# Optimization experiments

Hardware: AMD Instinct MI355X
Metric: run time of the kernel (lower is better)

## Reference

```python
import jax, jax.numpy as jnp
import numpy as np

NEG_INF = jnp.finfo(jnp.float32).min


def setup_inputs() -> dict:
    key = jax.random.key(0)
    ks = jax.random.split(key, 8)
    B, C, V = 64, 2048, 256
    ART = 2048
    D = C + ART        # 4096, classifier input
    F = 4096           # feature_size
    OUT = 1000         # out_channels
    x = jax.random.normal(ks[0], (B, C, V), dtype=jnp.float32)
    x_art = jax.random.normal(ks[1], (B, ART, V), dtype=jnp.float32)
    list_length = jax.random.randint(ks[2], (B,), 1, V + 1, dtype=jnp.int32)
    w1 = jax.random.normal(ks[3], (D, F), dtype=jnp.float32) * 0.02
    b1 = jnp.zeros((F,), dtype=jnp.float32)
    w2 = jax.random.normal(ks[4], (F, F), dtype=jnp.float32) * 0.02
    b2 = jnp.zeros((F,), dtype=jnp.float32)
    w3 = jax.random.normal(ks[5], (F, OUT), dtype=jnp.float32) * 0.02
    b3 = jnp.zeros((OUT,), dtype=jnp.float32)
    return {"x": x, "x_art": x_art, "list_length": list_length,
            "w1": w1, "b1": b1, "w2": w2, "b2": b2, "w3": w3, "b3": b3}


def reference(x, x_art, list_length, w1, b1, w2, b2, w3, b3):
    # x: [B, C, V], x_art: [B, ART, V] -> feats [B, V, C+ART]
    feats = jnp.concatenate((jnp.swapaxes(x, 1, 2), jnp.swapaxes(x_art, 1, 2)), axis=-1)
    B, V, D = feats.shape
    # Ragged max over views: view 0 is always included in the torch loop,
    # so effective length = max(list_length, 1).
    lens = jnp.maximum(list_length, 1)
    mask = jnp.arange(V, dtype=jnp.int32)[None, :] < lens[:, None]  # [B, V]
    pooled = jnp.max(jnp.where(mask[:, :, None], feats, NEG_INF), axis=1)  # [B, D]
    # Classifier MLP (dropout is identity at inference)
    h = jax.nn.relu(pooled @ w1 + b1)
    h = jax.nn.relu(h @ w2 + b2)
    return h @ w3 + b3
```

## Files before the change

### kernel.cpp

```cpp
#include <hip/hip_runtime.h>
#include <cfloat>

#define BB 64
#define CC 2048
#define AR 2048
#define DD 4096
#define VV 256
#define FF 4096
#define OO 1000

__global__ __launch_bounds__(256) void pool_kernel(
    const float* __restrict__ x, const float* __restrict__ xart,
    const int* __restrict__ ll, float* __restrict__ pooledT)
{
    int waveId = (blockIdx.x * 256 + threadIdx.x) >> 6;
    int lane   = threadIdx.x & 63;
    int row0   = waveId * 32;
    int b  = row0 >> 12;
    int d0 = row0 & 4095;
    int len = ll[b];
    if (len < 1) len = 1;
    const float* base = (d0 < CC)
        ? (x    + ((size_t)b * CC + d0)        * VV)
        : (xart + ((size_t)b * AR + (d0 - CC)) * VV);
    int v0  = lane * 4;
    int rem = len - v0;

    for (int r = 0; r < 32; r += 4) {
        const float* s = base + (size_t)r * VV;
        float m0 = -FLT_MAX, m1 = -FLT_MAX, m2 = -FLT_MAX, m3 = -FLT_MAX;
        if (rem > 0) {
            float4 a0 = *(const float4*)(s + v0);
            float4 a1 = *(const float4*)(s + VV + v0);
            float4 a2 = *(const float4*)(s + 2 * VV + v0);
            float4 a3 = *(const float4*)(s + 3 * VV + v0);
            m0 = a0.x; m1 = a1.x; m2 = a2.x; m3 = a3.x;
            if (rem > 1) { m0 = fmaxf(m0, a0.y); m1 = fmaxf(m1, a1.y);
                           m2 = fmaxf(m2, a2.y); m3 = fmaxf(m3, a3.y); }
            if (rem > 2) { m0 = fmaxf(m0, a0.z); m1 = fmaxf(m1, a1.z);
                           m2 = fmaxf(m2, a2.z); m3 = fmaxf(m3, a3.z); }
            if (rem > 3) { m0 = fmaxf(m0, a0.w); m1 = fmaxf(m1, a1.w);
                           m2 = fmaxf(m2, a2.w); m3 = fmaxf(m3, a3.w); }
        }
        #pragma unroll
        for (int off = 32; off > 0; off >>= 1) {
            m0 = fmaxf(m0, __shfl_xor(m0, off, 64));
            m1 = fmaxf(m1, __shfl_xor(m1, off, 64));
            m2 = fmaxf(m2, __shfl_xor(m2, off, 64));
            m3 = fmaxf(m3, __shfl_xor(m3, off, 64));
        }
        float wv = m0;
        if (lane == 1) wv = m1;
        else if (lane == 2) wv = m2;
        else if (lane == 3) wv = m3;
        if (lane < 4)
            pooledT[(size_t)(d0 + r + lane) * 64 + b] = wv;
    }
}

__global__ __launch_bounds__(256) void gemm_partial(
    const float* __restrict__ P, const float* __restrict__ W,
    float* __restrict__ part, int F, int kchunk)
{
    __shared__ float lds_p[16][64];
    __shared__ float lds_w[16][128];
    int t  = threadIdx.x;
    int tx = t & 15, ty = t >> 4;
    int f0 = blockIdx.x * 128;
    int k0 = blockIdx.y * kchunk;
    int stages = kchunk >> 4;
    int c1 = f0 + tx * 4;
    int c2 = f0 + 64 + tx * 4;
    bool v2 = (c2 + 3 < F) || (c2 + 4 == F);

    float acc[4][8];
    #pragma unroll
    for (int i = 0; i < 4; ++i)
        #pragma unroll
        for (int j = 0; j < 8; ++j) acc[i][j] = 0.f;

    int k = k0 + ty;
    float4 pv  = *(const float4*)(P + (size_t)k * 64 + tx * 4);
    const float* wr = W + (size_t)k * F;
    float4 wv0 = *(const float4*)(wr + c1);
    float4 wv1;
    if (v2) wv1 = *(const float4*)(wr + c2);
    else {
        wv1.x = (c2     < F) ? wr[c2]     : 0.f;
        wv1.y = (c2 + 1 < F) ? wr[c2 + 1] : 0.f;
        wv1.z = (c2 + 2 < F) ? wr[c2 + 2] : 0.f;
        wv1.w = (c2 + 3 < F) ? wr[c2 + 3] : 0.f;
    }

    for (int s = 0; s < stages; ++s) {
        __syncthreads();
        *(float4*)&lds_p[ty][tx * 4]      = pv;
        *(float4*)&lds_w[ty][tx * 4]      = wv0;
        *(float4*)&lds_w[ty][64 + tx * 4] = wv1;
        __syncthreads();
        if (s + 1 < stages) {
            int kn = k0 + (s + 1) * 16 + ty;
            pv = *(const float4*)(P + (size_t)kn * 64 + tx * 4);
            const float* wrn = W + (size_t)kn * F;
            wv0 = *(const float4*)(wrn + c1);
            if (v2) wv1 = *(const float4*)(wrn + c2);
            else {
                wv1.x = (c2     < F) ? wrn[c2]     : 0.f;
                wv1.y = (c2 + 1 < F) ? wrn[c2 + 1] : 0.f;
                wv1.z = (c2 + 2 < F) ? wrn[c2 + 2] : 0.f;
                wv1.w = (c2 + 3 < F) ? wrn[c2 + 3] : 0.f;
            }
        }
        #pragma unroll
        for (int kk = 0; kk < 16; ++kk) {
            float4 p4 = *(const float4*)&lds_p[kk][ty * 4];
            float4 wa = *(const float4*)&lds_w[kk][tx * 4];
            float4 wb = *(const float4*)&lds_w[kk][64 + tx * 4];
            #pragma unroll
            for (int i = 0; i < 4; ++i) {
                float pi = (i == 0) ? p4.x : (i == 1) ? p4.y : (i == 2) ? p4.z : p4.w;
                acc[i][0] += pi * wa.x;  acc[i][1] += pi * wa.y;
                acc[i][2] += pi * wa.z;  acc[i][3] += pi * wa.w;
                acc[i][4] += pi * wb.x;  acc[i][5] += pi * wb.y;
                acc[i][6] += pi * wb.z;  acc[i][7] += pi * wb.w;
            }
        }
    }

    float* dst = part + (size_t)(blockIdx.y * 64) * F;
    #pragma unroll
    for (int i = 0; i < 4; ++i) {
        float* r = dst + (size_t)(ty * 4 + i) * F;
        *(float4*)(r + c1) = make_float4(acc[i][0], acc[i][1], acc[i][2], acc[i][3]);
        if (v2)
            *(float4*)(r + c2) = make_float4(acc[i][4], acc[i][5], acc[i][6], acc[i][7]);
        else {
            if (c2     < F) r[c2]     = acc[i][4];
            if (c2 + 1 < F) r[c2 + 1] = acc[i][5];
            if (c2 + 2 < F) r[c2 + 2] = acc[i][6];
            if (c2 + 3 < F) r[c2 + 3] = acc[i][7];
        }
    }
}

__global__ __launch_bounds__(256) void reduce_bias_relu_T(
    const float* __restrict__ part, const float* __restrict__ bias,
    float* __restrict__ outT, int nchunk, int F)
{
    __shared__ float lds[64 * 17];
    int t  = threadIdx.x;
    int f0 = blockIdx.x * 16;
    int fl = t & 15;
    int ty = t >> 4;
    float bv = bias[f0 + fl];
    float acc[4];
    #pragma unroll
    for (int j = 0; j < 4; ++j) acc[j] = bv;
    for (int c = 0; c < nchunk; ++c) {
        const float* p = part + ((size_t)c * 64) * F + f0 + fl;
        #pragma unroll
        for (int j = 0; j < 4; ++j) {
            int b = j * 16 + ty;
            acc[j] += p[(size_t)b * F];
        }
    }
    #pragma unroll
    for (int j = 0; j < 4; ++j) {
        int b = j * 16 + ty;
        lds[b * 17 + fl] = fmaxf(acc[j], 0.f);
    }
    __syncthreads();
    #pragma unroll
    for (int j = 0; j < 4; ++j) {
        int idx = j * 256 + t;
        int f = idx >> 6;
        int b = idx & 63;
        outT[(size_t)(f0 + f) * 64 + b] = lds[b * 17 + f];
    }
}

__global__ __launch_bounds__(256) void reduce_out_kernel(
    const float* __restrict__ part, const float* __restrict__ bias,
    float* __restrict__ out, int nchunk)
{
    int idx = blockIdx.x * 256 + threadIdx.x;
    if (idx >= BB * OO) return;
    int b = idx / OO, f = idx - b * OO;
    float v = bias[f];
    const float* p = part + (size_t)b * OO + f;
    #pragma unroll 8
    for (int c = 0; c < nchunk; ++c)
        v += p[(size_t)c * 64 * OO];
    out[idx] = v;
}

extern "C" void kernel_launch(void* const* d_in, const int* in_sizes, int n_in,
                              void* d_out, int out_size, void* d_ws, size_t ws_size,
                              hipStream_t stream) {
    const float* x    = (const float*)d_in[0];
    const float* xart = (const float*)d_in[1];
    const int*   ll   = (const int*)d_in[2];
    const float* w1   = (const float*)d_in[3];
    const float* b1   = (const float*)d_in[4];
    const float* w2   = (const float*)d_in[5];
    const float* b2   = (const float*)d_in[6];
    const float* w3   = (const float*)d_in[7];
    const float* b3   = (const float*)d_in[8];
    float* out = (float*)d_out;

    float* pooledT = (float*)d_ws;
    float* h1T     = pooledT + (size_t)DD * 64;
    float* h2T     = h1T     + (size_t)FF * 64;
    float* part    = h2T     + (size_t)FF * 64;

    size_t actBytes = (size_t)(DD + FF + FF) * 64 * sizeof(float);
    size_t avail    = (ws_size > actBytes) ? ws_size - actBytes : 0;
    size_t plane1   = (size_t)64 * FF * sizeof(float);
    int nk1 = 8;
    if (avail >= 32 * plane1)      nk1 = 32;
    else if (avail >= 16 * plane1) nk1 = 16;
    size_t plane3 = (size_t)64 * OO * sizeof(float);
    int nk3 = (avail >= 64 * plane3) ? 64 : 32;
    int kchunk1 = DD / nk1;
    int kchunk3 = FF / nk3;

    pool_kernel<<<2048, 256, 0, stream>>>(x, xart, ll, pooledT);

    gemm_partial<<<dim3(32, nk1), 256, 0, stream>>>(pooledT, w1, part, FF, kchunk1);
    reduce_bias_relu_T<<<FF / 16, 256, 0, stream>>>(part, b1, h1T, nk1, FF);

    gemm_partial<<<dim3(32, nk1), 256, 0, stream>>>(h1T, w2, part, FF, kchunk1);
    reduce_bias_relu_T<<<FF / 16, 256, 0, stream>>>(part, b2, h2T, nk1, FF);

    gemm_partial<<<dim3(8, nk3), 256, 0, stream>>>(h2T, w3, part, OO, kchunk3);
    reduce_out_kernel<<<(BB * OO + 255) / 256, 256, 0, stream>>>(part, b3, out, nk3);
}
```

Baseline: 417.5 us.

## Replace LDS-tiled GEMM with register-only skinny GEMM, lane per batch row

```diff
diff --git a/kernel.cpp b/kernel.cpp
--- a/kernel.cpp
+++ b/kernel.cpp
@@ -58,88 +58,74 @@
     }
 }
 
-__global__ __launch_bounds__(256) void gemm_partial(
-    const float* __restrict__ P, const float* __restrict__ W,
-    float* __restrict__ part, int F, int kchunk)
-{
-    __shared__ float lds_p[16][64];
-    __shared__ float lds_w[16][128];
-    int t  = threadIdx.x;
-    int tx = t & 15, ty = t >> 4;
-    int f0 = blockIdx.x * 128;
-    int k0 = blockIdx.y * kchunk;
-    int stages = kchunk >> 4;
-    int c1 = f0 + tx * 4;
-    int c2 = f0 + 64 + tx * 4;
-    bool v2 = (c2 + 3 < F) || (c2 + 4 == F);
-
-    float acc[4][8];
+#define FT 32
+
+__global__ __launch_bounds__(256, 4) void gemm_skinny(
+    const float* __restrict__ P,
+    const float* __restrict__ W,
+    float* __restrict__ part,
+    int F, int kchunk)
+{
+    int winb = threadIdx.x >> 6;
+    int lane = threadIdx.x & 63;
+    int f0   = (blockIdx.x * 4 + winb) * FT;
+    int k0   = blockIdx.y * kchunk;
+
+    const float* prow = P + (size_t)k0 * 64 + lane;
+    const float* wrow = W + (size_t)k0 * F + f0;
+
+    float acc[FT];
     #pragma unroll
-    for (int i = 0; i < 4; ++i)
-        #pragma unroll
-        for (int j = 0; j < 8; ++j) acc[i][j] = 0.f;
-
-    int k = k0 + ty;
-    float4 pv  = *(const float4*)(P + (size_t)k * 64 + tx * 4);
-    const float* wr = W + (size_t)k * F;
-    float4 wv0 = *(const float4*)(wr + c1);
-    float4 wv1;
-    if (v2) wv1 = *(const float4*)(wr + c2);
-    else {
-        wv1.x = (c2     < F) ? wr[c2]     : 0.f;
-        wv1.y = (c2 + 1 < F) ? wr[c2 + 1] : 0.f;
-        wv1.z = (c2 + 2 < F) ? wr[c2 + 2] : 0.f;
-        wv1.w = (c2 + 3 < F) ? wr[c2 + 3] : 0.f;
-    }
-
-    for (int s = 0; s < stages; ++s) {
-        __syncthreads();
-        *(float4*)&lds_p[ty][tx * 4]      = pv;
-        *(float4*)&lds_w[ty][tx * 4]      = wv0;
-        *(float4*)&lds_w[ty][64 + tx * 4] = wv1;
-        __syncthreads();
-        if (s + 1 < stages) {
-            int kn = k0 + (s + 1) * 16 + ty;
-            pv = *(const float4*)(P + (size_t)kn * 64 + tx * 4);
-            const float* wrn = W + (size_t)kn * F;
-            wv0 = *(const float4*)(wrn + c1);
-            if (v2) wv1 = *(const float4*)(wrn + c2);
-            else {
-                wv1.x = (c2     < F) ? wrn[c2]     : 0.f;
-                wv1.y = (c2 + 1 < F) ? wrn[c2 + 1] : 0.f;
-                wv1.z = (c2 + 2 < F) ? wrn[c2 + 2] : 0.f;
-                wv1.w = (c2 + 3 < F) ? wrn[c2 + 3] : 0.f;
+    for (int j = 0; j < FT; ++j) acc[j] = 0.f;
+
+    if (f0 + FT <= F) {
+        float pv = prow[0];
+        float4 wv[FT / 4];
+        #pragma unroll
+        for (int q = 0; q < FT / 4; ++q)
+            wv[q] = *(const float4*)(wrow + 4 * q);
+
+        for (int k = 0; k < kchunk - 1; ++k) {
+            float pn = prow[(size_t)(k + 1) * 64];
+            const float* wr = wrow + (size_t)(k + 1) * F;
+            float4 wn[FT / 4];
+            #pragma unroll
+            for (int q = 0; q < FT / 4; ++q)
+                wn[q] = *(const float4*)(wr + 4 * q);
+            #pragma unroll
+            for (int q = 0; q < FT / 4; ++q) {
+                acc[4 * q + 0] += pv * wv[q].x;
+                acc[4 * q + 1] += pv * wv[q].y;
+                acc[4 * q + 2] += pv * wv[q].z;
+                acc[4 * q + 3] += pv * wv[q].w;
             }
-        }
-        #pragma unroll
-        for (int kk = 0; kk < 16; ++kk) {
-            float4 p4 = *(const float4*)&lds_p[kk][ty * 4];
-            float4 wa = *(const float4*)&lds_w[kk][tx * 4];
-            float4 wb = *(const float4*)&lds_w[kk][64 + tx * 4];
-            #pragma unroll
-            for (int i = 0; i < 4; ++i) {
-                float pi = (i == 0) ? p4.x : (i == 1) ? p4.y : (i == 2) ? p4.z : p4.w;
-                acc[i][0] += pi * wa.x;  acc[i][1] += pi * wa.y;
-                acc[i][2] += pi * wa.z;  acc[i][3] += pi * wa.w;
-                acc[i][4] += pi * wb.x;  acc[i][5] += pi * wb.y;
-                acc[i][6] += pi * wb.z;  acc[i][7] += pi * wb.w;
-            }
-        }
-    }
-
-    float* dst = part + (size_t)(blockIdx.y * 64) * F;
-    #pragma unroll
-    for (int i = 0; i < 4; ++i) {
-        float* r = dst + (size_t)(ty * 4 + i) * F;
-        *(float4*)(r + c1) = make_float4(acc[i][0], acc[i][1], acc[i][2], acc[i][3]);
-        if (v2)
-            *(float4*)(r + c2) = make_float4(acc[i][4], acc[i][5], acc[i][6], acc[i][7]);
-        else {
-            if (c2     < F) r[c2]     = acc[i][4];
-            if (c2 + 1 < F) r[c2 + 1] = acc[i][5];
-            if (c2 + 2 < F) r[c2 + 2] = acc[i][6];
-            if (c2 + 3 < F) r[c2 + 3] = acc[i][7];
-        }
+            pv = pn;
+            #pragma unroll
+            for (int q = 0; q < FT / 4; ++q) wv[q] = wn[q];
+        }
+        #pragma unroll
+        for (int q = 0; q < FT / 4; ++q) {
+            acc[4 * q + 0] += pv * wv[q].x;
+            acc[4 * q + 1] += pv * wv[q].y;
+            acc[4 * q + 2] += pv * wv[q].z;
+            acc[4 * q + 3] += pv * wv[q].w;
+        }
+        float* dst = part + ((size_t)blockIdx.y * F + f0) * 64 + lane;
+        #pragma unroll
+        for (int j = 0; j < FT; ++j)
+            dst[(size_t)j * 64] = acc[j];
+    } else {
+        for (int k = 0; k < kchunk; ++k) {
+            float pv = prow[(size_t)k * 64];
+            const float* wr = wrow + (size_t)k * F;
+            #pragma unroll
+            for (int j = 0; j < FT; ++j)
+                if (f0 + j < F) acc[j] += pv * wr[j];
+        }
+        float* dst = part + ((size_t)blockIdx.y * F + f0) * 64 + lane;
+        #pragma unroll
+        for (int j = 0; j < FT; ++j)
+            if (f0 + j < F) dst[(size_t)j * 64] = acc[j];
     }
 }
 
@@ -147,36 +133,16 @@
     const float* __restrict__ part, const float* __restrict__ bias,
     float* __restrict__ outT, int nchunk, int F)
 {
-    __shared__ float lds[64 * 17];
-    int t  = threadIdx.x;
-    int f0 = blockIdx.x * 16;
-    int fl = t & 15;
-    int ty = t >> 4;
-    float bv = bias[f0 + fl];
-    float acc[4];
-    #pragma unroll
-    for (int j = 0; j < 4; ++j) acc[j] = bv;
-    for (int c = 0; c < nchunk; ++c) {
-        const float* p = part + ((size_t)c * 64) * F + f0 + fl;
-        #pragma unroll
-        for (int j = 0; j < 4; ++j) {
-            int b = j * 16 + ty;
-            acc[j] += p[(size_t)b * F];
-        }
-    }
-    #pragma unroll
-    for (int j = 0; j < 4; ++j) {
-        int b = j * 16 + ty;
-        lds[b * 17 + fl] = fmaxf(acc[j], 0.f);
-    }
-    __syncthreads();
-    #pragma unroll
-    for (int j = 0; j < 4; ++j) {
-        int idx = j * 256 + t;
-        int f = idx >> 6;
-        int b = idx & 63;
-        outT[(size_t)(f0 + f) * 64 + b] = lds[b * 17 + f];
-    }
+    int lane = threadIdx.x & 63;
+    int fl   = threadIdx.x >> 6;
+    int f    = blockIdx.x * 4 + fl;
+    float acc = bias[f];
+    const float* p = part + (size_t)f * 64 + lane;
+    size_t stride = (size_t)F * 64;
+    #pragma unroll 8
+    for (int c = 0; c < nchunk; ++c)
+        acc += p[(size_t)c * stride];
+    outT[(size_t)f * 64 + lane] = fmaxf(acc, 0.f);
 }
 
 __global__ __launch_bounds__(256) void reduce_out_kernel(
@@ -184,14 +150,15 @@
     float* __restrict__ out, int nchunk)
 {
     int idx = blockIdx.x * 256 + threadIdx.x;
-    if (idx >= BB * OO) return;
-    int b = idx / OO, f = idx - b * OO;
+    if (idx >= OO * 64) return;
+    int f = idx >> 6, b = idx & 63;
     float v = bias[f];
-    const float* p = part + (size_t)b * OO + f;
+    const float* p = part + (size_t)f * 64 + b;
+    size_t stride = (size_t)OO * 64;
     #pragma unroll 8
     for (int c = 0; c < nchunk; ++c)
-        v += p[(size_t)c * 64 * OO];
-    out[idx] = v;
+        v += p[(size_t)c * stride];
+    out[(size_t)b * OO + f] = v;
 }
 
 extern "C" void kernel_launch(void* const* d_in, const int* in_sizes, int n_in,
@@ -226,12 +193,12 @@
 
     pool_kernel<<<2048, 256, 0, stream>>>(x, xart, ll, pooledT);
 
-    gemm_partial<<<dim3(32, nk1), 256, 0, stream>>>(pooledT, w1, part, FF, kchunk1);
-    reduce_bias_relu_T<<<FF / 16, 256, 0, stream>>>(part, b1, h1T, nk1, FF);
-
-    gemm_partial<<<dim3(32, nk1), 256, 0, stream>>>(h1T, w2, part, FF, kchunk1);
-    reduce_bias_relu_T<<<FF / 16, 256, 0, stream>>>(part, b2, h2T, nk1, FF);
-
-    gemm_partial<<<dim3(8, nk3), 256, 0, stream>>>(h2T, w3, part, OO, kchunk3);
+    gemm_skinny<<<dim3(FF / (FT * 4), nk1), 256, 0, stream>>>(pooledT, w1, part, FF, kchunk1);
+    reduce_bias_relu_T<<<FF / 4, 256, 0, stream>>>(part, b1, h1T, nk1, FF);
+
+    gemm_skinny<<<dim3(FF / (FT * 4), nk1), 256, 0, stream>>>(h1T, w2, part, FF, kchunk1);
+    reduce_bias_relu_T<<<FF / 4, 256, 0, stream>>>(part, b2, h2T, nk1, FF);
+
+    gemm_skinny<<<dim3(8, nk3), 256, 0, stream>>>(h2T, w3, part, OO, kchunk3);
     reduce_out_kernel<<<(BB * OO + 255) / 256, 256, 0, stream>>>(part, b3, out, nk3);
 }
```

Measured after the change: 744.8 us. +78.4%, slower.
